# Optimization experiments

Measured on AMD Instinct MI355X. Metric: run time of the kernel, lower is better.

Reference implementation:

```python
import jax, jax.numpy as jnp
import numpy as np

KERNEL_SIZE = 15  # matches init kwarg


def setup_inputs() -> dict:
    key = jax.random.key(0)
    k1, k2 = jax.random.split(key)
    B, T, C, H, W = 1, 8, 3, 96, 96
    K2 = KERNEL_SIZE * KERNEL_SIZE
    data = jax.random.normal(k1, (B, T, C, H, W), dtype=jnp.float32)
    kernels = jax.random.uniform(k2, (B, T, K2, C, H, W), dtype=jnp.float32)
    return {"data": data, "kernels": kernels}


def reference(data, kernels):
    # data:    [B, T, C, H, W]
    # kernels: [B, T, K*K, C, H, W]
    K = KERNEL_SIZE
    p = K // 2
    H, W = data.shape[-2], data.shape[-1]
    # zero-pad spatial dims (matches F.pad with default mode='constant')
    dp = jnp.pad(data, ((0, 0), (0, 0), (0, 0), (p, p), (p, p)))
    # shift-stack: tap order is i (row offset) major, j (col offset) minor,
    # matching the torch double loop.  stack axis=2 -> [B, T, K*K, C, H, W]
    img_stack = jnp.stack(
        [dp[..., i:i + H, j:j + W] for i in range(K) for j in range(K)],
        axis=2,
    )
    # per-pixel dynamic kernel: multiply and reduce over the K*K taps
    pred_burst = jnp.sum(kernels * img_stack, axis=2)  # [B, T, C, H, W]
    return pred_burst
```

## Files before the change

kernel.cpp:

```cpp
#include <hip/hip_runtime.h>


constexpr int K   = 15;
constexpr int P   = 7;
constexpr int H   = 96;
constexpr int W   = 96;
constexpr int C   = 3;
constexpr int T   = 8;
constexpr int HW  = H * W;
constexpr int K2  = K * K;
constexpr int QW  = W / 4;
constexpr int QPP = H * QW;
constexpr int NQ  = T * C * QPP;
constexpr int BLK = 64;
constexpr int NBLK = NQ / BLK;

__global__ __launch_bounds__(BLK) void kpn_kernel(
    const float* __restrict__ data,
    const float* __restrict__ kern,
    float* __restrict__ out)
{
    const int q = blockIdx.x * BLK + threadIdx.x;

    const int w4    = q % QW;
    const int rem   = q / QW;
    const int h     = rem % H;
    const int plane = rem / H;
    const int t     = plane / C;
    const int c     = plane % C;
    const int wbase = w4 * 4;

    const float* __restrict__ dplane = data + plane * HW;
    const float* __restrict__ kbase =
        kern + ((size_t)(t * K2) * C + (size_t)c) * HW + (size_t)h * W + wbase;
    const size_t kstride = (size_t)C * HW;

    int  colc[K + 3];
    bool cval[K + 3];
    #pragma unroll
    for (int m = 0; m < K + 3; ++m) {
        const int col = wbase - P + m;
        cval[m] = (col >= 0) && (col < W);
        colc[m] = (col < 0) ? 0 : ((col >= W) ? (W - 1) : col);
    }

    float4 acc = make_float4(0.f, 0.f, 0.f, 0.f);

    for (int i = 0; i < K; ++i) {
        const int srow = h + i - P;
        const bool rv  = (srow >= 0) && (srow < H);
        const float* __restrict__ drow = dplane + (rv ? srow : 0) * W;

        float dwin[K + 3];
        #pragma unroll
        for (int m = 0; m < K + 3; ++m) {
            const float v = drow[colc[m]];
            dwin[m] = (rv && cval[m]) ? v : 0.f;
        }

        const float* __restrict__ krow = kbase + (size_t)(i * K) * kstride;

        float4 kv[K];
        #pragma unroll
        for (int j = 0; j < K; ++j) {
            kv[j] = *reinterpret_cast<const float4*>(krow + (size_t)j * kstride);
        }
        #pragma unroll
        for (int j = 0; j < K; ++j) {
            acc.x += kv[j].x * dwin[j + 0];
            acc.y += kv[j].y * dwin[j + 1];
            acc.z += kv[j].z * dwin[j + 2];
            acc.w += kv[j].w * dwin[j + 3];
        }
    }

    *reinterpret_cast<float4*>(out + (size_t)plane * HW + (size_t)h * W + wbase) = acc;
}

extern "C" void kernel_launch(void* const* d_in, const int* in_sizes, int n_in,
                              void* d_out, int out_size, void* d_ws, size_t ws_size,
                              hipStream_t stream) {
    const float* data = (const float*)d_in[0];
    const float* kern = (const float*)d_in[1];
    float* out        = (float*)d_out;
    hipLaunchKernelGGL(kpn_kernel, dim3(NBLK), dim3(BLK), 0, stream,
                       data, kern, out);
}
```

Measured before the change: 291.8 us.

## Split tap-row reduction across waves with workspace partials and a reduce pass

The per-pixel dynamic convolution is split across the 15 kernel rows. Each wave computes one tap row's partial sums for an 8x96 tile, with 12 pixels per thread, and writes them to a workspace buffer. A second kernel then sums the 15 partials. This exposes many more waves to hide memory latency on the large kernel-tensor stream, at the cost of an extra write and read of the partials and a second launch. If the workspace is too small, a fused single-pass kernel with far fewer waves is used instead.

New measurement: 288.5 us. No clear change (-1.1%).

```diff
diff --git a/kernel.cpp b/kernel.cpp
--- a/kernel.cpp
+++ b/kernel.cpp
@@ -1,80 +1,124 @@
 #include <hip/hip_runtime.h>
 
 
-constexpr int K   = 15;
-constexpr int P   = 7;
-constexpr int H   = 96;
-constexpr int W   = 96;
-constexpr int C   = 3;
-constexpr int T   = 8;
-constexpr int HW  = H * W;
-constexpr int K2  = K * K;
-constexpr int QW  = W / 4;
-constexpr int QPP = H * QW;
-constexpr int NQ  = T * C * QPP;
-constexpr int BLK = 64;
-constexpr int NBLK = NQ / BLK;
+constexpr int K    = 15;
+constexpr int P    = 7;
+constexpr int H    = 96;
+constexpr int W    = 96;
+constexpr int C    = 3;
+constexpr int T    = 8;
+constexpr int HW   = H * W;
+constexpr int K2   = K * K;
+constexpr int NP   = T * C;
+constexpr int NE   = NP * HW;
+constexpr int PXT  = 12;
+constexpr int ROWS_PER_WAVE = 8;
+constexpr int TILES = NP * (H / ROWS_PER_WAVE);
+constexpr int NWAVE1 = TILES * K;
+constexpr int BLK1 = 256;
+constexpr int NBLK1 = NWAVE1 / 4;
+constexpr size_t PART_FLOATS = (size_t)K * NE;
+constexpr size_t PART_BYTES  = PART_FLOATS * 4;
 
-__global__ __launch_bounds__(BLK) void kpn_kernel(
+__device__ __forceinline__ void tap_row_accum(
+    const float* __restrict__ data, const float* __restrict__ kern,
+    int plane, int t, int c, int r, int cg, int i,
+    float4& a0, float4& a1, float4& a2)
+{
+    const int srow = r + i - P;
+    const bool rv  = (srow >= 0) && (srow < H);
+    const float* __restrict__ drow = data + plane * HW + (rv ? srow : 0) * W;
+
+    float dwin[26];
+    #pragma unroll
+    for (int m = 0; m < 26; ++m) {
+        const int col = cg - P + m;
+        const int cc  = (col < 0) ? 0 : ((col >= W) ? (W - 1) : col);
+        const float v = drow[cc];
+        dwin[m] = (rv && col >= 0 && col < W) ? v : 0.f;
+    }
+
+    const float* __restrict__ kptr =
+        kern + ((size_t)((t * K2 + i * K) * C + c)) * HW + (size_t)r * W + cg;
+
+    #pragma unroll
+    for (int j = 0; j < K; ++j) {
+        const float4* __restrict__ kp =
+            reinterpret_cast<const float4*>(kptr + (size_t)j * (C * HW));
+        const float4 k0 = kp[0];
+        const float4 k1 = kp[1];
+        const float4 k2 = kp[2];
+        a0.x += k0.x * dwin[j + 0];  a0.y += k0.y * dwin[j + 1];
+        a0.z += k0.z * dwin[j + 2];  a0.w += k0.w * dwin[j + 3];
+        a1.x += k1.x * dwin[j + 4];  a1.y += k1.y * dwin[j + 5];
+        a1.z += k1.z * dwin[j + 6];  a1.w += k1.w * dwin[j + 7];
+        a2.x += k2.x * dwin[j + 8];  a2.y += k2.y * dwin[j + 9];
+        a2.z += k2.z * dwin[j + 10]; a2.w += k2.w * dwin[j + 11];
+    }
+}
+
+__global__ __launch_bounds__(BLK1, 4) void kpn_part(
+    const float* __restrict__ data,
+    const float* __restrict__ kern,
+    float* __restrict__ part)
+{
+    const int w    = blockIdx.x * 4 + (threadIdx.x >> 6);
+    const int lane = threadIdx.x & 63;
+    const int i    = w / TILES;
+    const int tile = w % TILES;
+    const int plane = tile / (H / ROWS_PER_WAVE);
+    const int rb    = tile % (H / ROWS_PER_WAVE);
+    const int t = plane / C;
+    const int c = plane % C;
+    const int r  = rb * ROWS_PER_WAVE + (lane >> 3);
+    const int cg = (lane & 7) * PXT;
+
+    float4 a0 = make_float4(0.f,0.f,0.f,0.f);
+    float4 a1 = a0, a2 = a0;
+    tap_row_accum(data, kern, plane, t, c, r, cg, i, a0, a1, a2);
+
+    float* pp = part + (size_t)i * NE + (size_t)plane * HW + (size_t)r * W + cg;
+    reinterpret_cast<float4*>(pp)[0] = a0;
+    reinterpret_cast<float4*>(pp)[1] = a1;
+    reinterpret_cast<float4*>(pp)[2] = a2;
+}
+
+__global__ __launch_bounds__(256) void kpn_reduce(
+    const float4* __restrict__ part, float4* __restrict__ out)
+{
+    const int e = blockIdx.x * 256 + threadIdx.x;
+    float4 s = make_float4(0.f,0.f,0.f,0.f);
+    #pragma unroll
+    for (int i = 0; i < K; ++i) {
+        const float4 p = part[(size_t)i * (NE / 4) + e];
+        s.x += p.x; s.y += p.y; s.z += p.z; s.w += p.w;
+    }
+    out[e] = s;
+}
+
+__global__ __launch_bounds__(BLK1) void kpn_fused(
     const float* __restrict__ data,
     const float* __restrict__ kern,
     float* __restrict__ out)
 {
-    const int q = blockIdx.x * BLK + threadIdx.x;
+    const int w    = blockIdx.x * 4 + (threadIdx.x >> 6);
+    const int lane = threadIdx.x & 63;
+    const int plane = w / (H / ROWS_PER_WAVE);
+    const int rb    = w % (H / ROWS_PER_WAVE);
+    const int t = plane / C;
+    const int c = plane % C;
+    const int r  = rb * ROWS_PER_WAVE + (lane >> 3);
+    const int cg = (lane & 7) * PXT;
 
-    const int w4    = q % QW;
-    const int rem   = q / QW;
-    const int h     = rem % H;
-    const int plane = rem / H;
-    const int t     = plane / C;
-    const int c     = plane % C;
-    const int wbase = w4 * 4;
+    float4 a0 = make_float4(0.f,0.f,0.f,0.f);
+    float4 a1 = a0, a2 = a0;
+    for (int i = 0; i < K; ++i)
+        tap_row_accum(data, kern, plane, t, c, r, cg, i, a0, a1, a2);
 
-    const float* __restrict__ dplane = data + plane * HW;
-    const float* __restrict__ kbase =
-        kern + ((size_t)(t * K2) * C + (size_t)c) * HW + (size_t)h * W + wbase;
-    const size_t kstride = (size_t)C * HW;
-
-    int  colc[K + 3];
-    bool cval[K + 3];
-    #pragma unroll
-    for (int m = 0; m < K + 3; ++m) {
-        const int col = wbase - P + m;
-        cval[m] = (col >= 0) && (col < W);
-        colc[m] = (col < 0) ? 0 : ((col >= W) ? (W - 1) : col);
-    }
-
-    float4 acc = make_float4(0.f, 0.f, 0.f, 0.f);
-
-    for (int i = 0; i < K; ++i) {
-        const int srow = h + i - P;
-        const bool rv  = (srow >= 0) && (srow < H);
-        const float* __restrict__ drow = dplane + (rv ? srow : 0) * W;
-
-        float dwin[K + 3];
-        #pragma unroll
-        for (int m = 0; m < K + 3; ++m) {
-            const float v = drow[colc[m]];
-            dwin[m] = (rv && cval[m]) ? v : 0.f;
-        }
-
-        const float* __restrict__ krow = kbase + (size_t)(i * K) * kstride;
-
-        float4 kv[K];
-        #pragma unroll
-        for (int j = 0; j < K; ++j) {
-            kv[j] = *reinterpret_cast<const float4*>(krow + (size_t)j * kstride);
-        }
-        #pragma unroll
-        for (int j = 0; j < K; ++j) {
-            acc.x += kv[j].x * dwin[j + 0];
-            acc.y += kv[j].y * dwin[j + 1];
-            acc.z += kv[j].z * dwin[j + 2];
-            acc.w += kv[j].w * dwin[j + 3];
-        }
-    }
-
-    *reinterpret_cast<float4*>(out + (size_t)plane * HW + (size_t)h * W + wbase) = acc;
+    float* op = out + (size_t)plane * HW + (size_t)r * W + cg;
+    reinterpret_cast<float4*>(op)[0] = a0;
+    reinterpret_cast<float4*>(op)[1] = a1;
+    reinterpret_cast<float4*>(op)[2] = a2;
 }
 
 extern "C" void kernel_launch(void* const* d_in, const int* in_sizes, int n_in,
@@ -83,6 +127,15 @@
     const float* data = (const float*)d_in[0];
     const float* kern = (const float*)d_in[1];
     float* out        = (float*)d_out;
-    hipLaunchKernelGGL(kpn_kernel, dim3(NBLK), dim3(BLK), 0, stream,
-                       data, kern, out);
+
+    if (ws_size >= PART_BYTES) {
+        float* part = (float*)d_ws;
+        hipLaunchKernelGGL(kpn_part, dim3(NBLK1), dim3(BLK1), 0, stream,
+                           data, kern, part);
+        hipLaunchKernelGGL(kpn_reduce, dim3(NE / 4 / 256), dim3(256), 0, stream,
+                           (const float4*)part, (float4*)out);
+    } else {
+        hipLaunchKernelGGL(kpn_fused, dim3(TILES / 4), dim3(BLK1), 0, stream,
+                           data, kern, out);
+    }
 }
```

## Split kernel-row reduction across waves with workspace partials and reduce pass

Applied to the files above, without the earlier changes.

Splits the 15 kernel rows into independent waves, each writing a partial float4 sum to a workspace buffer, then runs a second kernel that sums the 15 partials. The point is more memory-level parallelism and occupancy on this bandwidth-bound dynamic-filter op, where the old version had only about 4.6K threads each looping over all rows. It also retiles threads into 8x32 wave tiles with 256-thread blocks. The cost is an extra write and read of a 15x output-sized partial buffer plus a second launch. If the workspace is too small it falls back to a single fused kernel.

Measured after the change: 277.2 us. 5.0% less time.

```diff
diff --git a/kernel.cpp b/kernel.cpp
--- a/kernel.cpp
+++ b/kernel.cpp
@@ -9,61 +9,117 @@
 constexpr int T   = 8;
 constexpr int HW  = H * W;
 constexpr int K2  = K * K;
-constexpr int QW  = W / 4;
-constexpr int QPP = H * QW;
-constexpr int NQ  = T * C * QPP;
-constexpr int BLK = 64;
-constexpr int NBLK = NQ / BLK;
+constexpr int NP  = T * C;
+constexpr int NE  = NP * HW;
+constexpr int TR  = 8;
+constexpr int TC  = 32;
+constexpr int TPP = (H / TR) * (W / TC);
+constexpr int TILES = NP * TPP;
+constexpr int NWAVES = TILES * K;
+constexpr int NBLK1  = NWAVES / 4;
+constexpr size_t PART_BYTES = (size_t)K * NE * 4;
 
-__global__ __launch_bounds__(BLK) void kpn_kernel(
+__global__ __launch_bounds__(256, 4) void kpn_part(
+    const float* __restrict__ data,
+    const float* __restrict__ kern,
+    float* __restrict__ part)
+{
+    const int w    = blockIdx.x * 4 + (threadIdx.x >> 6);
+    const int lane = threadIdx.x & 63;
+    const int i    = w / TILES;
+    const int tile = w % TILES;
+    const int plane = tile / TPP;
+    const int tp    = tile % TPP;
+    const int rg    = tp / (W / TC);
+    const int cgp   = tp % (W / TC);
+    const int r     = rg * TR + (lane >> 3);
+    const int col   = cgp * TC + (lane & 7) * 4;
+    const int t = plane / C;
+    const int c = plane % C;
+
+    const float* __restrict__ kptr =
+        kern + ((size_t)((t * K2 + i * K) * C + c)) * HW + (size_t)r * W + col;
+    float4 kv[K];
+    #pragma unroll
+    for (int j = 0; j < K; ++j) {
+        kv[j] = *reinterpret_cast<const float4*>(kptr + (size_t)j * (C * HW));
+    }
+
+    const int srow = r + i - P;
+    const bool rv  = (srow >= 0) && (srow < H);
+    const float* __restrict__ drow = data + plane * HW + (rv ? srow : 0) * W;
+    float dwin[K + 3];
+    #pragma unroll
+    for (int m = 0; m < K + 3; ++m) {
+        const int cc  = col - P + m;
+        const int ccc = (cc < 0) ? 0 : ((cc >= W) ? (W - 1) : cc);
+        const float v = drow[ccc];
+        dwin[m] = (rv && cc >= 0 && cc < W) ? v : 0.f;
+    }
+
+    float4 acc = make_float4(0.f, 0.f, 0.f, 0.f);
+    #pragma unroll
+    for (int j = 0; j < K; ++j) {
+        acc.x += kv[j].x * dwin[j + 0];
+        acc.y += kv[j].y * dwin[j + 1];
+        acc.z += kv[j].z * dwin[j + 2];
+        acc.w += kv[j].w * dwin[j + 3];
+    }
+
+    float* pp = part + (size_t)i * NE + (size_t)plane * HW + (size_t)r * W + col;
+    *reinterpret_cast<float4*>(pp) = acc;
+}
+
+__global__ __launch_bounds__(256) void kpn_reduce(
+    const float4* __restrict__ part, float4* __restrict__ out)
+{
+    const int e = blockIdx.x * 256 + threadIdx.x;
+    float4 p[K];
+    #pragma unroll
+    for (int i = 0; i < K; ++i) p[i] = part[(size_t)i * (NE / 4) + e];
+    float4 s = make_float4(0.f, 0.f, 0.f, 0.f);
+    #pragma unroll
+    for (int i = 0; i < K; ++i) {
+        s.x += p[i].x; s.y += p[i].y; s.z += p[i].z; s.w += p[i].w;
+    }
+    out[e] = s;
+}
+
+__global__ __launch_bounds__(256, 4) void kpn_fused(
     const float* __restrict__ data,
     const float* __restrict__ kern,
     float* __restrict__ out)
 {
-    const int q = blockIdx.x * BLK + threadIdx.x;
-
-    const int w4    = q % QW;
-    const int rem   = q / QW;
-    const int h     = rem % H;
-    const int plane = rem / H;
-    const int t     = plane / C;
-    const int c     = plane % C;
-    const int wbase = w4 * 4;
-
-    const float* __restrict__ dplane = data + plane * HW;
-    const float* __restrict__ kbase =
-        kern + ((size_t)(t * K2) * C + (size_t)c) * HW + (size_t)h * W + wbase;
-    const size_t kstride = (size_t)C * HW;
-
-    int  colc[K + 3];
-    bool cval[K + 3];
-    #pragma unroll
-    for (int m = 0; m < K + 3; ++m) {
-        const int col = wbase - P + m;
-        cval[m] = (col >= 0) && (col < W);
-        colc[m] = (col < 0) ? 0 : ((col >= W) ? (W - 1) : col);
-    }
+    const int w    = blockIdx.x * 4 + (threadIdx.x >> 6);
+    const int lane = threadIdx.x & 63;
+    const int plane = w / TPP;
+    const int tp    = w % TPP;
+    const int rg    = tp / (W / TC);
+    const int cgp   = tp % (W / TC);
+    const int r     = rg * TR + (lane >> 3);
+    const int col   = cgp * TC + (lane & 7) * 4;
+    const int t = plane / C;
+    const int c = plane % C;
 
     float4 acc = make_float4(0.f, 0.f, 0.f, 0.f);
+    for (int i = 0; i < K; ++i) {
+        const float* __restrict__ kptr =
+            kern + ((size_t)((t * K2 + i * K) * C + c)) * HW + (size_t)r * W + col;
+        float4 kv[K];
+        #pragma unroll
+        for (int j = 0; j < K; ++j)
+            kv[j] = *reinterpret_cast<const float4*>(kptr + (size_t)j * (C * HW));
 
-    for (int i = 0; i < K; ++i) {
-        const int srow = h + i - P;
+        const int srow = r + i - P;
         const bool rv  = (srow >= 0) && (srow < H);
-        const float* __restrict__ drow = dplane + (rv ? srow : 0) * W;
-
+        const float* __restrict__ drow = data + plane * HW + (rv ? srow : 0) * W;
         float dwin[K + 3];
         #pragma unroll
         for (int m = 0; m < K + 3; ++m) {
-            const float v = drow[colc[m]];
-            dwin[m] = (rv && cval[m]) ? v : 0.f;
-        }
-
-        const float* __restrict__ krow = kbase + (size_t)(i * K) * kstride;
-
-        float4 kv[K];
-        #pragma unroll
-        for (int j = 0; j < K; ++j) {
-            kv[j] = *reinterpret_cast<const float4*>(krow + (size_t)j * kstride);
+            const int cc  = col - P + m;
+            const int ccc = (cc < 0) ? 0 : ((cc >= W) ? (W - 1) : cc);
+            const float v = drow[ccc];
+            dwin[m] = (rv && cc >= 0 && cc < W) ? v : 0.f;
         }
         #pragma unroll
         for (int j = 0; j < K; ++j) {
@@ -73,8 +129,8 @@
             acc.w += kv[j].w * dwin[j + 3];
         }
     }
-
-    *reinterpret_cast<float4*>(out + (size_t)plane * HW + (size_t)h * W + wbase) = acc;
+    float* op = out + (size_t)plane * HW + (size_t)r * W + col;
+    *reinterpret_cast<float4*>(op) = acc;
 }
 
 extern "C" void kernel_launch(void* const* d_in, const int* in_sizes, int n_in,
@@ -83,6 +139,15 @@
     const float* data = (const float*)d_in[0];
     const float* kern = (const float*)d_in[1];
     float* out        = (float*)d_out;
-    hipLaunchKernelGGL(kpn_kernel, dim3(NBLK), dim3(BLK), 0, stream,
-                       data, kern, out);
+
+    if (ws_size >= PART_BYTES) {
+        float* part = (float*)d_ws;
+        hipLaunchKernelGGL(kpn_part, dim3(NBLK1), dim3(256), 0, stream,
+                           data, kern, part);
+        hipLaunchKernelGGL(kpn_reduce, dim3(NE / 4 / 256), dim3(256), 0, stream,
+                           (const float4*)part, (float4*)out);
+    } else {
+        hipLaunchKernelGGL(kpn_fused, dim3(TILES / 4), dim3(256), 0, stream,
+                           data, kern, out);
+    }
 }
```

## Split tap reduction across wave groups with partial sums and reduce pass

Applied to the files above, without the earlier changes.

Splits the 225 kernel taps into 9 groups of 25. Each 64-thread wave handles one group over a 16-row tile, loads kernel weights with nontemporal loads through a double-buffered register pipeline, and writes partial sums to workspace. A second kernel adds the 9 partials. This exposes more parallelism and more memory-level overlap for what is a bandwidth-bound stream over the large kernel tensor, at the cost of extra partial-sum traffic and a second launch. A fused fallback with 256-thread blocks runs when the workspace is too small.

New measurement: 294.1 us. Within noise of the previous version (+0.8%).

```diff
diff --git a/kernel.cpp b/kernel.cpp
--- a/kernel.cpp
+++ b/kernel.cpp
@@ -1,69 +1,157 @@
 #include <hip/hip_runtime.h>
 
 
-constexpr int K   = 15;
-constexpr int P   = 7;
-constexpr int H   = 96;
-constexpr int W   = 96;
-constexpr int C   = 3;
-constexpr int T   = 8;
-constexpr int HW  = H * W;
-constexpr int K2  = K * K;
-constexpr int QW  = W / 4;
-constexpr int QPP = H * QW;
-constexpr int NQ  = T * C * QPP;
-constexpr int BLK = 64;
-constexpr int NBLK = NQ / BLK;
+typedef float vf4 __attribute__((ext_vector_type(4)));
 
-__global__ __launch_bounds__(BLK) void kpn_kernel(
+constexpr int K  = 15;
+constexpr int P  = 7;
+constexpr int H  = 96;
+constexpr int W  = 96;
+constexpr int C  = 3;
+constexpr int T  = 8;
+constexpr int HW = H * W;
+constexpr int K2 = K * K;
+constexpr int NP = T * C;
+constexpr int NE = NP * HW;
+constexpr size_t CHW = (size_t)C * HW;
+constexpr int SR   = 16;
+constexpr int SPP  = H / SR;
+constexpr int TILES = NP * SPP;
+constexpr int KGRP = 9;
+constexpr int KPG  = 25;
+constexpr int NWAVES = TILES * KGRP;
+constexpr int QL = (SR * W) / (64 * 4);
+constexpr size_t PART_BYTES = (size_t)KGRP * NE * 4;
+
+__device__ __forceinline__ vf4 nt4(const float* p) {
+    return __builtin_nontemporal_load(reinterpret_cast<const vf4*>(p));
+}
+
+__global__ __launch_bounds__(64) void kpn_part(
+    const float* __restrict__ data,
+    const float* __restrict__ kern,
+    float* __restrict__ part)
+{
+    const int lane = threadIdx.x;
+    const int w    = blockIdx.x;
+    const int kg   = w / TILES;
+    const int tile = w % TILES;
+    const int plane = tile / SPP;
+    const int s     = tile % SPP;
+    const int t  = plane / C;
+    const int c  = plane % C;
+    const int r0 = s * SR;
+
+    int qrow[QL], qcol[QL];
+    #pragma unroll
+    for (int q = 0; q < QL; ++q) {
+        const int flat = (q * 64 + lane) * 4;
+        qrow[q] = flat / W;
+        qcol[q] = flat % W;
+    }
+
+    const float* __restrict__ dpl = data + plane * HW;
+    const float* __restrict__ kbase =
+        kern + (size_t)(t * K2) * CHW + (size_t)c * HW + (size_t)r0 * W + lane * 4;
+    const int k0 = kg * KPG;
+
+    float acc[QL][4];
+    #pragma unroll
+    for (int q = 0; q < QL; ++q)
+        #pragma unroll
+        for (int e = 0; e < 4; ++e) acc[q][e] = 0.f;
+
+    auto load_stage = [&](vf4 (&buf)[QL], int k) {
+        const float* p = kbase + (size_t)k * CHW;
+        #pragma unroll
+        for (int q = 0; q < QL; ++q) buf[q] = nt4(p + q * 256);
+    };
+
+    auto consume = [&](vf4 (&buf)[QL], int k) {
+        const int i = k / K;
+        const int j = k % K;
+        #pragma unroll
+        for (int q = 0; q < QL; ++q) {
+            const int sr  = r0 + qrow[q] + i - P;
+            const bool rv = (sr >= 0) && (sr < H);
+            const float* __restrict__ drow = dpl + (rv ? sr : 0) * W;
+            #pragma unroll
+            for (int e = 0; e < 4; ++e) {
+                const int sc  = qcol[q] + e + j - P;
+                const bool cv = rv && (sc >= 0) && (sc < W);
+                const int scc = (sc < 0) ? 0 : ((sc >= W) ? (W - 1) : sc);
+                const float dv = drow[scc];
+                acc[q][e] += buf[q][e] * (cv ? dv : 0.f);
+            }
+        }
+    };
+
+    vf4 A[QL], B[QL];
+    load_stage(A, k0);
+    #pragma unroll 1
+    for (int u = 0; u < KPG - 1; u += 2) {
+        load_stage(B, k0 + u + 1);
+        consume(A, k0 + u);
+        load_stage(A, k0 + u + 2);
+        consume(B, k0 + u + 1);
+    }
+    consume(A, k0 + KPG - 1);
+
+    float* pp = part + (size_t)kg * NE + (size_t)plane * HW
+                     + (size_t)r0 * W + lane * 4;
+    #pragma unroll
+    for (int q = 0; q < QL; ++q) {
+        vf4 v = { acc[q][0], acc[q][1], acc[q][2], acc[q][3] };
+        __builtin_nontemporal_store(v, reinterpret_cast<vf4*>(pp + q * 256));
+    }
+}
+
+__global__ __launch_bounds__(256) void kpn_reduce(
+    const float* __restrict__ part, float* __restrict__ out)
+{
+    const int e4 = blockIdx.x * 256 + threadIdx.x;
+    const float* p = part + (size_t)e4 * 4;
+    vf4 sum = {0.f, 0.f, 0.f, 0.f};
+    #pragma unroll
+    for (int g = 0; g < KGRP; ++g) {
+        sum += nt4(p + (size_t)g * NE);
+    }
+    __builtin_nontemporal_store(sum, reinterpret_cast<vf4*>(out + (size_t)e4 * 4));
+}
+
+__global__ __launch_bounds__(256, 4) void kpn_fused(
     const float* __restrict__ data,
     const float* __restrict__ kern,
     float* __restrict__ out)
 {
-    const int q = blockIdx.x * BLK + threadIdx.x;
-
-    const int w4    = q % QW;
-    const int rem   = q / QW;
-    const int h     = rem % H;
+    const int gq   = blockIdx.x * 256 + threadIdx.x;
+    const int w4   = gq % (W / 4);
+    const int rem  = gq / (W / 4);
+    const int h    = rem % H;
     const int plane = rem / H;
-    const int t     = plane / C;
-    const int c     = plane % C;
-    const int wbase = w4 * 4;
-
-    const float* __restrict__ dplane = data + plane * HW;
-    const float* __restrict__ kbase =
-        kern + ((size_t)(t * K2) * C + (size_t)c) * HW + (size_t)h * W + wbase;
-    const size_t kstride = (size_t)C * HW;
-
-    int  colc[K + 3];
-    bool cval[K + 3];
-    #pragma unroll
-    for (int m = 0; m < K + 3; ++m) {
-        const int col = wbase - P + m;
-        cval[m] = (col >= 0) && (col < W);
-        colc[m] = (col < 0) ? 0 : ((col >= W) ? (W - 1) : col);
-    }
+    const int t = plane / C;
+    const int c = plane % C;
+    const int col = w4 * 4;
 
     float4 acc = make_float4(0.f, 0.f, 0.f, 0.f);
+    for (int i = 0; i < K; ++i) {
+        const float* __restrict__ kptr =
+            kern + ((size_t)((t * K2 + i * K) * C + c)) * HW + (size_t)h * W + col;
+        float4 kv[K];
+        #pragma unroll
+        for (int j = 0; j < K; ++j)
+            kv[j] = *reinterpret_cast<const float4*>(kptr + (size_t)j * CHW);
 
-    for (int i = 0; i < K; ++i) {
         const int srow = h + i - P;
         const bool rv  = (srow >= 0) && (srow < H);
-        const float* __restrict__ drow = dplane + (rv ? srow : 0) * W;
-
+        const float* __restrict__ drow = data + plane * HW + (rv ? srow : 0) * W;
         float dwin[K + 3];
         #pragma unroll
         for (int m = 0; m < K + 3; ++m) {
-            const float v = drow[colc[m]];
-            dwin[m] = (rv && cval[m]) ? v : 0.f;
-        }
-
-        const float* __restrict__ krow = kbase + (size_t)(i * K) * kstride;
-
-        float4 kv[K];
-        #pragma unroll
-        for (int j = 0; j < K; ++j) {
-            kv[j] = *reinterpret_cast<const float4*>(krow + (size_t)j * kstride);
+            const int cc  = col - P + m;
+            const int ccc = (cc < 0) ? 0 : ((cc >= W) ? (W - 1) : cc);
+            const float v = drow[ccc];
+            dwin[m] = (rv && cc >= 0 && cc < W) ? v : 0.f;
         }
         #pragma unroll
         for (int j = 0; j < K; ++j) {
@@ -73,8 +161,8 @@
             acc.w += kv[j].w * dwin[j + 3];
         }
     }
-
-    *reinterpret_cast<float4*>(out + (size_t)plane * HW + (size_t)h * W + wbase) = acc;
+    float* op = out + (size_t)plane * HW + (size_t)h * W + col;
+    *reinterpret_cast<float4*>(op) = acc;
 }
 
 extern "C" void kernel_launch(void* const* d_in, const int* in_sizes, int n_in,
@@ -83,6 +171,15 @@
     const float* data = (const float*)d_in[0];
     const float* kern = (const float*)d_in[1];
     float* out        = (float*)d_out;
-    hipLaunchKernelGGL(kpn_kernel, dim3(NBLK), dim3(BLK), 0, stream,
-                       data, kern, out);
+
+    if (ws_size >= PART_BYTES) {
+        float* part = (float*)d_ws;
+        hipLaunchKernelGGL(kpn_part, dim3(NWAVES), dim3(64), 0, stream,
+                           data, kern, part);
+        hipLaunchKernelGGL(kpn_reduce, dim3(NE / 4 / 256), dim3(256), 0, stream,
+                           part, out);
+    } else {
+        hipLaunchKernelGGL(kpn_fused, dim3(NE / 4 / 256), dim3(256), 0, stream,
+                           data, kern, out);
+    }
 }
```
